# Optimization experiments

Hardware: AMD Instinct MI355X
Metric: run time of the kernel (lower is better)

Reference implementation:

```python
import jax, jax.numpy as jnp
import numpy as np

B, T, D = 16, 512, 1024
H = 4
DH = D // H
L = 2
FF = 4 * D
MAX_CORR = 3
THRESH = 0.3
EPS = 1e-5


def _ln(x, g, b):
    mu = x.mean(-1, keepdims=True)
    var = ((x - mu) ** 2).mean(-1, keepdims=True)
    return (x - mu) / jnp.sqrt(var + EPS) * g + b


def _prm(x, Wqkv, bqkv, Wo, bo, ln1_g, ln1_b, W1, b1, W2, b2, ln2_g, ln2_b,
         rh_W1, rh_b1, rh_W2, rh_b2):
    # PyTorch TransformerEncoder (post-LN, relu, dropout off) with causal mask
    Bs, Ts, _ = x.shape
    causal = jnp.triu(jnp.ones((Ts, Ts), dtype=bool), k=1)  # True = masked
    for l in range(L):
        qkv = x @ Wqkv[l].T + bqkv[l]  # (B,T,3D)
        q, k, v = jnp.split(qkv, 3, axis=-1)
        q = q.reshape(Bs, Ts, H, DH)
        k = k.reshape(Bs, Ts, H, DH)
        v = v.reshape(Bs, Ts, H, DH)
        scores = jnp.einsum('bthd,bshd->bhts', q, k) / jnp.sqrt(jnp.float32(DH))
        scores = jnp.where(causal[None, None], -jnp.inf, scores)
        attn = jax.nn.softmax(scores, axis=-1)
        o = jnp.einsum('bhts,bshd->bthd', attn, v).reshape(Bs, Ts, D)
        o = o @ Wo[l].T + bo[l]
        x = _ln(x + o, ln1_g[l], ln1_b[l])
        h = jax.nn.relu(x @ W1[l].T + b1[l]) @ W2[l].T + b2[l]
        x = _ln(x + h, ln2_g[l], ln2_b[l])
    r = jax.nn.relu(x @ rh_W1.T + rh_b1) @ rh_W2.T + rh_b2  # (B,T,1)
    return jax.nn.sigmoid(r[..., 0])  # (B,T)


def setup_inputs() -> dict:
    key = jax.random.key(0)
    ks = jax.random.split(key, 24)
    s = 0.02
    inp = {
        'chain': jax.random.normal(ks[0], (B, T, D), jnp.float32),
        'Wqkv': jax.random.normal(ks[1], (L, 3 * D, D), jnp.float32) * s,
        'bqkv': jnp.zeros((L, 3 * D), jnp.float32),
        'Wo': jax.random.normal(ks[2], (L, D, D), jnp.float32) * s,
        'bo': jnp.zeros((L, D), jnp.float32),
        'ln1_g': jnp.ones((L, D), jnp.float32),
        'ln1_b': jnp.zeros((L, D), jnp.float32),
        'W1': jax.random.normal(ks[3], (L, FF, D), jnp.float32) * s,
        'b1': jnp.zeros((L, FF), jnp.float32),
        'W2': jax.random.normal(ks[4], (L, D, FF), jnp.float32) * s,
        'b2': jnp.zeros((L, D), jnp.float32),
        'ln2_g': jnp.ones((L, D), jnp.float32),
        'ln2_b': jnp.zeros((L, D), jnp.float32),
        'rh_W1': jax.random.normal(ks[5], (D // 2, D), jnp.float32) * s,
        'rh_b1': jnp.zeros((D // 2,), jnp.float32),
        'rh_W2': jax.random.normal(ks[6], (1, D // 2), jnp.float32) * s,
        'rh_b2': jnp.full((1,), -1.0, jnp.float32),  # bias so some scores fall below threshold
        'cor_W1': jax.random.normal(ks[7], (2 * D, 2 * D), jnp.float32) * s,
        'cor_b1': jnp.zeros((2 * D,), jnp.float32),
        'cor_W2': jax.random.normal(ks[8], (D, 2 * D), jnp.float32) * s,
        'cor_b2': jnp.zeros((D,), jnp.float32),
    }
    return inp


def reference(chain, Wqkv, bqkv, Wo, bo, ln1_g, ln1_b, W1, b1, W2, b2,
              ln2_g, ln2_b, rh_W1, rh_b1, rh_W2, rh_b2,
              cor_W1, cor_b1, cor_W2, cor_b2):
    prm = lambda x: _prm(x, Wqkv, bqkv, Wo, bo, ln1_g, ln1_b, W1, b1, W2, b2,
                         ln2_g, ln2_b, rh_W1, rh_b1, rh_W2, rh_b2)
    scores0 = prm(chain)
    corrected = chain
    counts = jnp.zeros((B,), jnp.int32)
    offs = jnp.array([-1, 0, 1], jnp.int32)
    tpos = jnp.arange(T)
    for _ in range(MAX_CORR):
        s = prm(corrected)  # (B,T)
        below = s < THRESH
        has_bad = below.any(axis=-1)  # (B,)
        # worst = first argmin among below-threshold steps (matches torch argmin over gathered)
        w = jnp.argmin(jnp.where(below, s, jnp.inf), axis=-1)  # (B,)
        # context: mean over valid window [w-1, w+2)
        idxs = w[:, None] + offs  # (B,3)
        valid = (idxs >= 0) & (idxs < T)
        gathered = jnp.take_along_axis(corrected, jnp.clip(idxs, 0, T - 1)[..., None], axis=1)  # (B,3,D)
        ctx = (gathered * valid[..., None]).sum(1) / valid.sum(1, keepdims=True)  # (B,D)
        cur = jnp.take_along_axis(corrected, jnp.broadcast_to(w[:, None, None], (B, 1, D)), axis=1)[:, 0]  # (B,D)
        cinp = jnp.concatenate([cur, ctx], axis=-1)  # (B,2D)
        new_step = jax.nn.relu(cinp @ cor_W1.T + cor_b1) @ cor_W2.T + cor_b2  # (B,D)
        sel = (tpos[None, :] == w[:, None]) & has_bad[:, None]  # (B,T)
        corrected = jnp.where(sel[..., None], new_step[:, None, :], corrected)
        counts = counts + has_bad.astype(jnp.int32)
    final_scores = prm(corrected)
    improved = final_scores.mean(-1) > scores0.mean(-1)
    return corrected, counts, final_scores, improved
```

## Files before the change

### kernel.cpp

```cpp
#include <hip/hip_runtime.h>
#include <math.h>

#define B_ 16
#define T_ 512
#define D_ 1024
#define H_ 4
#define DH_ 256
#define FF_ 4096
#define M_ (B_*T_)
#define THRESH_ 0.3f
#define EPS_ 1e-5f

#define GF_RELU 1
#define GF_RES  2
#define GF_OUTBF16 4
#define GF_SPLITV 8

typedef unsigned short ushort_t;
typedef unsigned int uint_t;

using s16x8 = __attribute__((ext_vector_type(8))) short;
using f32x4 = __attribute__((ext_vector_type(4))) float;
using f32x16 = __attribute__((ext_vector_type(16))) float;

typedef const __attribute__((address_space(1))) void* gas_ptr;
typedef __attribute__((address_space(3))) void* lds_ptr;

static __device__ __forceinline__ ushort_t f2bf(float f) {
  uint_t x = __float_as_uint(f);
  return (ushort_t)((x + 0x7FFFu + ((x >> 16) & 1u)) >> 16);
}
static __device__ __forceinline__ float bf2f(ushort_t u) {
  return __uint_as_float(((uint_t)u) << 16);
}

__global__ __launch_bounds__(256)
void cvt_f32_bf16(const float* __restrict__ in, ushort_t* __restrict__ out, int n)
{
  const int i = (blockIdx.x * 256 + threadIdx.x) << 2;
  if (i >= n) return;
  const float4 v = *(const float4*)(in + i);
  ushort4 o;
  o.x = f2bf(v.x); o.y = f2bf(v.y); o.z = f2bf(v.z); o.w = f2bf(v.w);
  *(ushort4*)(out + i) = o;
}

__global__ __launch_bounds__(256)
void gemm_bf16(const ushort_t* __restrict__ A, const ushort_t* __restrict__ Bt,
               const float* __restrict__ bias, const ushort_t* __restrict__ res,
               float* __restrict__ outF, ushort_t* __restrict__ outB,
               ushort_t* __restrict__ vt,
               int M, int N, int K, int flags)
{
  __shared__ ushort_t As[128 * 32];
  __shared__ ushort_t Bs[128 * 32];
  const int npn = gridDim.x;
  const int pid = blockIdx.y * npn + blockIdx.x;
  const int group = 8 * npn;
  const int first_m = (pid / group) * 8;
  const int pid_m = first_m + (pid % 8);
  const int pid_n = (pid % group) >> 3;
  const int n0 = pid_n << 7;
  const int m0 = pid_m << 7;

  const int tid = threadIdx.x;
  const int wv = tid >> 6, ln = tid & 63;
  const int wm = (wv >> 1) << 6;
  const int wn = (wv & 1) << 6;
  const int col32 = ln & 31, l5 = ln >> 5;

  f32x16 acc[2][2] = {};

  const ushort_t* ga = A + (size_t)(m0 + wv * 16 + (ln >> 2)) * K + ((ln & 3) << 3);
  const ushort_t* gb = Bt + (size_t)(n0 + wv * 16 + (ln >> 2)) * K + ((ln & 3) << 3);
  ushort_t* lA = &As[wv * 512];
  ushort_t* lB = &Bs[wv * 512];

  for (int k0 = 0; k0 < K; k0 += 32) {
    __builtin_amdgcn_global_load_lds((gas_ptr)(const void*)ga,
                                     (lds_ptr)(void*)lA, 16, 0, 0);
    __builtin_amdgcn_global_load_lds((gas_ptr)(const void*)(ga + (size_t)64 * K),
                                     (lds_ptr)(void*)(lA + 2048), 16, 0, 0);
    __builtin_amdgcn_global_load_lds((gas_ptr)(const void*)gb,
                                     (lds_ptr)(void*)lB, 16, 0, 0);
    __builtin_amdgcn_global_load_lds((gas_ptr)(const void*)(gb + (size_t)64 * K),
                                     (lds_ptr)(void*)(lB + 2048), 16, 0, 0);
    ga += 32; gb += 32;
    __syncthreads();
    s16x8 af[2][2], bfr[2][2];
#pragma unroll
    for (int mt = 0; mt < 2; ++mt)
#pragma unroll
      for (int kh = 0; kh < 2; ++kh)
        af[mt][kh] = *(const s16x8*)(&As[(wm + mt * 32 + col32) * 32
                                         + kh * 16 + l5 * 8]);
#pragma unroll
    for (int nt = 0; nt < 2; ++nt)
#pragma unroll
      for (int kh = 0; kh < 2; ++kh)
        bfr[nt][kh] = *(const s16x8*)(&Bs[(wn + nt * 32 + col32) * 32
                                          + kh * 16 + l5 * 8]);
#pragma unroll
    for (int kh = 0; kh < 2; ++kh)
#pragma unroll
      for (int mt = 0; mt < 2; ++mt)
#pragma unroll
        for (int nt = 0; nt < 2; ++nt)
          acc[mt][nt] = __builtin_amdgcn_mfma_f32_32x32x16_bf16(
              af[mt][kh], bfr[nt][kh], acc[mt][nt], 0, 0, 0);
    __syncthreads();
  }

#pragma unroll
  for (int mt = 0; mt < 2; ++mt)
#pragma unroll
    for (int nt = 0; nt < 2; ++nt) {
      const int c = n0 + wn + nt * 32 + col32;
      const float bb = bias[c];
      const bool isV = (flags & GF_SPLITV) && (c >= 2048);
#pragma unroll
      for (int reg = 0; reg < 16; ++reg) {
        const int row = m0 + wm + mt * 32 + (reg & 3) + ((reg >> 2) << 3)
                        + (l5 << 2);
        float v = acc[mt][nt][reg] + bb;
        const size_t idx = (size_t)row * N + c;
        if (flags & GF_RES) v += bf2f(res[idx]);
        if (flags & GF_RELU) v = fmaxf(v, 0.f);
        if (isV) {
          const int t = row & 511, bb2 = row >> 9;
          const int hh = (c - 2048) >> 8, d = (c - 2048) & 255;
          vt[(((size_t)(bb2 * 4 + hh) * 16 + (t >> 5)) << 13) + d * 32 + (t & 31)]
              = f2bf(v);
        } else if (flags & GF_OUTBF16) outB[idx] = f2bf(v);
        else outF[idx] = v;
      }
    }
}

__global__ __launch_bounds__(256)
void flash_attn(const ushort_t* __restrict__ qkv, const ushort_t* __restrict__ vtg,
                ushort_t* __restrict__ ao)
{
  __shared__ ushort_t Ks[2][8 * 64 * 32];
  __shared__ ushort_t Vs[2][2 * 256 * 32];
  __shared__ ushort_t Ph[4][16][80];
  __shared__ ushort_t Pl[4][16][80];
  const int qt = (int)gridDim.x - 1 - blockIdx.x;
  const int t0 = qt << 6;
  const int bh = blockIdx.y;
  const int b = bh >> 2, h = bh & 3;
  const int nIter = qt + 1;
  const int tid = threadIdx.x;
  const int wv = tid >> 6, ln = tid & 63;
  const int lrow = ln & 15, quad = ln >> 4;

  s16x8 qf[8];
  {
    const ushort_t* qrow = qkv + (size_t)(b * T_ + t0 + wv * 16 + lrow) * 3072
                           + h * 256 + quad * 8;
#pragma unroll
    for (int kc = 0; kc < 8; ++kc)
      qf[kc] = *(const s16x8*)(qrow + kc * 32);
  }

  const ushort_t* kg = qkv + (size_t)(b * T_) * 3072 + 1024 + h * 256;
  const ushort_t* vg = vtg + (size_t)bh * 131072;

  auto issue_k = [&](int i, int buf) {
#pragma unroll
    for (int iss = 0; iss < 8; ++iss) {
      const int R = 128 * wv + 16 * iss + (ln >> 2);
      const ushort_t* g = kg + (size_t)(64 * i + (R & 63)) * 3072
                          + (R >> 6) * 32 + ((ln & 3) << 3);
      ushort_t* l = &Ks[buf][(128 * wv + 16 * iss) * 32];
      __builtin_amdgcn_global_load_lds((gas_ptr)(const void*)g,
                                       (lds_ptr)(void*)l, 16, 0, 0);
    }
  };
  auto issue_v = [&](int i, int buf) {
#pragma unroll
    for (int iss = 0; iss < 8; ++iss) {
      const ushort_t* g = vg + (size_t)i * 16384 + wv * 4096 + iss * 512 + ln * 8;
      ushort_t* l = &Vs[buf][wv * 4096 + iss * 512];
      __builtin_amdgcn_global_load_lds((gas_ptr)(const void*)g,
                                       (lds_ptr)(void*)l, 16, 0, 0);
    }
  };

  issue_k(0, 0);
  issue_v(0, 0);

  f32x4 o[16] = {};
  float Mx[4], L[4];
#pragma unroll
  for (int r = 0; r < 4; ++r) { Mx[r] = -3.0e38f; L[r] = 0.f; }

  for (int it = 0; it < nIter; ++it) {
    const int buf = it & 1;
    __syncthreads();
    if (it + 1 < nIter) { issue_k(it + 1, buf ^ 1); issue_v(it + 1, buf ^ 1); }

    f32x4 s[4] = {};
#pragma unroll
    for (int kc = 0; kc < 8; ++kc)
#pragma unroll
      for (int j = 0; j < 4; ++j) {
        const s16x8 bfv = *(const s16x8*)(&Ks[buf][(kc * 64 + 16 * j + lrow) * 32
                                                   + quad * 8]);
        s[j] = __builtin_amdgcn_mfma_f32_16x16x32_bf16(qf[kc], bfv, s[j], 0, 0, 0);
      }

    const bool diag = (it == qt);
#pragma unroll
    for (int j = 0; j < 4; ++j)
#pragma unroll
      for (int r = 0; r < 4; ++r) {
        float v = s[j][r] * 0.0625f;
        if (diag && (16 * j + lrow > 16 * wv + quad * 4 + r)) v = -INFINITY;
        s[j][r] = v;
      }

    float alpha[4];
#pragma unroll
    for (int r = 0; r < 4; ++r) {
      float m = fmaxf(fmaxf(s[0][r], s[1][r]), fmaxf(s[2][r], s[3][r]));
      m = fmaxf(m, __shfl_xor(m, 1));
      m = fmaxf(m, __shfl_xor(m, 2));
      m = fmaxf(m, __shfl_xor(m, 4));
      m = fmaxf(m, __shfl_xor(m, 8));
      const float mn = fmaxf(Mx[r], m);
      alpha[r] = __expf(Mx[r] - mn);
      Mx[r] = mn;
      float l = 0.f;
#pragma unroll
      for (int j = 0; j < 4; ++j) {
        const float p = __expf(s[j][r] - mn);
        s[j][r] = p;
        l += p;
      }
      l += __shfl_xor(l, 1);
      l += __shfl_xor(l, 2);
      l += __shfl_xor(l, 4);
      l += __shfl_xor(l, 8);
      L[r] = L[r] * alpha[r] + l;
    }

#pragma unroll
    for (int j = 0; j < 4; ++j)
#pragma unroll
      for (int r = 0; r < 4; ++r) {
        const float p = s[j][r];
        const ushort_t hi = f2bf(p);
        Ph[wv][quad * 4 + r][16 * j + lrow] = hi;
        Pl[wv][quad * 4 + r][16 * j + lrow] = f2bf(p - bf2f(hi));
      }
#pragma unroll
    for (int jd = 0; jd < 16; ++jd)
#pragma unroll
      for (int r = 0; r < 4; ++r)
        o[jd][r] *= alpha[r];

#pragma unroll
    for (int c = 0; c < 2; ++c) {
      const s16x8 ph = *(const s16x8*)(&Ph[wv][lrow][32 * c + quad * 8]);
      const s16x8 pl = *(const s16x8*)(&Pl[wv][lrow][32 * c + quad * 8]);
#pragma unroll
      for (int jd = 0; jd < 16; ++jd) {
        const s16x8 vb = *(const s16x8*)(&Vs[buf][(c * 256 + 16 * jd + lrow) * 32
                                                  + quad * 8]);
        o[jd] = __builtin_amdgcn_mfma_f32_16x16x32_bf16(ph, vb, o[jd], 0, 0, 0);
        o[jd] = __builtin_amdgcn_mfma_f32_16x16x32_bf16(pl, vb, o[jd], 0, 0, 0);
      }
    }
  }

  float inv[4];
#pragma unroll
  for (int r = 0; r < 4; ++r) inv[r] = 1.f / L[r];
  ushort_t* aob = ao + (size_t)(b * T_ + t0 + 16 * wv + quad * 4) * 1024 + h * 256;
#pragma unroll
  for (int jd = 0; jd < 16; ++jd)
#pragma unroll
    for (int r = 0; r < 4; ++r)
      aob[(size_t)r * 1024 + 16 * jd + lrow] = f2bf(o[jd][r] * inv[r]);
}

__global__ __launch_bounds__(256)
void gemm_bt(const float* __restrict__ A, const float* __restrict__ Bt,
             const float* __restrict__ bias, float* __restrict__ out,
             int M, int N, int K, int flags)
{
  __shared__ float As[16][68];
  __shared__ float Bs[16][68];
  const int n0 = blockIdx.x << 6;
  const int m0 = blockIdx.y << 6;
  const int tx = threadIdx.x, ty = threadIdx.y;
  const int tid = (ty << 4) + tx;
  const int lr = tid >> 2;
  const int lc = (tid & 3) << 2;
  float c[4][4] = {};
  for (int k0 = 0; k0 < K; k0 += 16) {
    float4 av = make_float4(0.f, 0.f, 0.f, 0.f);
    if (m0 + lr < M)
      av = *(const float4*)(A + (size_t)(m0 + lr) * K + k0 + lc);
    const float4 bv = *(const float4*)(Bt + (size_t)(n0 + lr) * K + k0 + lc);
    As[lc + 0][lr] = av.x; As[lc + 1][lr] = av.y;
    As[lc + 2][lr] = av.z; As[lc + 3][lr] = av.w;
    Bs[lc + 0][lr] = bv.x; Bs[lc + 1][lr] = bv.y;
    Bs[lc + 2][lr] = bv.z; Bs[lc + 3][lr] = bv.w;
    __syncthreads();
#pragma unroll
    for (int k = 0; k < 16; ++k) {
      const float4 a = *(const float4*)(&As[k][ty << 2]);
      const float4 b = *(const float4*)(&Bs[k][tx << 2]);
      c[0][0] += a.x*b.x; c[0][1] += a.x*b.y; c[0][2] += a.x*b.z; c[0][3] += a.x*b.w;
      c[1][0] += a.y*b.x; c[1][1] += a.y*b.y; c[1][2] += a.y*b.z; c[1][3] += a.y*b.w;
      c[2][0] += a.z*b.x; c[2][1] += a.z*b.y; c[2][2] += a.z*b.z; c[2][3] += a.z*b.w;
      c[3][0] += a.w*b.x; c[3][1] += a.w*b.y; c[3][2] += a.w*b.z; c[3][3] += a.w*b.w;
    }
    __syncthreads();
  }
  const int n = n0 + (tx << 2);
  const float4 bb = *(const float4*)(bias + n);
#pragma unroll
  for (int i = 0; i < 4; ++i) {
    const int m = m0 + (ty << 2) + i;
    if (m >= M) break;
    float4 v = make_float4(c[i][0] + bb.x, c[i][1] + bb.y,
                           c[i][2] + bb.z, c[i][3] + bb.w);
    if (flags & GF_RELU) {
      v.x = fmaxf(v.x, 0.f); v.y = fmaxf(v.y, 0.f);
      v.z = fmaxf(v.z, 0.f); v.w = fmaxf(v.w, 0.f);
    }
    *(float4*)(out + (size_t)m * N + n) = v;
  }
}

__global__ __launch_bounds__(256)
void layernorm_k(const float* __restrict__ in, const float* __restrict__ g,
                 const float* __restrict__ bta, ushort_t* __restrict__ outb)
{
  const int row = blockIdx.x;
  const int tid = threadIdx.x;
  const int wave = tid >> 6, lane = tid & 63;
  const float4 v = *(const float4*)(in + (size_t)row * D_ + (tid << 2));
  float s = v.x + v.y + v.z + v.w;
  float ss = v.x*v.x + v.y*v.y + v.z*v.z + v.w*v.w;
  for (int off = 32; off; off >>= 1) {
    s  += __shfl_down(s, off, 64);
    ss += __shfl_down(ss, off, 64);
  }
  __shared__ float ra[4], rb[4];
  if (!lane) { ra[wave] = s; rb[wave] = ss; }
  __syncthreads();
  s  = ra[0] + ra[1] + ra[2] + ra[3];
  ss = rb[0] + rb[1] + rb[2] + rb[3];
  const float mu = s * (1.f / (float)D_);
  const float var = ss * (1.f / (float)D_) - mu * mu;
  const float rstd = rsqrtf(var + EPS_);
  const float4 gv = *(const float4*)(g + (tid << 2));
  const float4 bv = *(const float4*)(bta + (tid << 2));
  ushort4 o;
  o.x = f2bf((v.x - mu) * rstd * gv.x + bv.x);
  o.y = f2bf((v.y - mu) * rstd * gv.y + bv.y);
  o.z = f2bf((v.z - mu) * rstd * gv.z + bv.z);
  o.w = f2bf((v.w - mu) * rstd * gv.w + bv.w);
  *(ushort4*)(outb + (size_t)row * D_ + (tid << 2)) = o;
}

__global__ __launch_bounds__(256)
void head2_sigmoid(const float* __restrict__ h1, const float* __restrict__ w2,
                   const float* __restrict__ b2, float* __restrict__ sout)
{
  const int tid = threadIdx.x;
  const int wave = tid >> 6, lane = tid & 63;
  const int m = (blockIdx.x << 2) + wave;
  const float* hr = h1 + (size_t)m * 512;
  float s = 0.f;
#pragma unroll
  for (int i = 0; i < 8; ++i) s += hr[i * 64 + lane] * w2[i * 64 + lane];
  for (int off = 32; off; off >>= 1) s += __shfl_down(s, off, 64);
  if (!lane) sout[m] = 1.f / (1.f + expf(-(s + b2[0])));
}

__global__ __launch_bounds__(256)
void select_worst(const float* __restrict__ s, int* __restrict__ w,
                  int* __restrict__ hasbad, int* __restrict__ counts)
{
  const int b = blockIdx.x, tid = threadIdx.x;
  const float* sr = s + b * T_;
  float bv = INFINITY; int bi = 0;
  for (int i = tid; i < T_; i += 256) {
    const float v = sr[i];
    const float cand = (v < THRESH_) ? v : INFINITY;
    if (cand < bv || (cand == bv && i < bi)) { bv = cand; bi = i; }
  }
  __shared__ float rv[256];
  __shared__ int ri[256];
  rv[tid] = bv; ri[tid] = bi;
  __syncthreads();
  for (int str = 128; str; str >>= 1) {
    if (tid < str) {
      const float v2 = rv[tid + str]; const int i2 = ri[tid + str];
      if (v2 < rv[tid] || (v2 == rv[tid] && i2 < ri[tid])) { rv[tid] = v2; ri[tid] = i2; }
    }
    __syncthreads();
  }
  if (!tid) {
    const int bad = (rv[0] < INFINITY) ? 1 : 0;
    w[b] = ri[0];
    hasbad[b] = bad;
    counts[b] += bad;
  }
}

__global__ __launch_bounds__(256)
void gather_cinp(const float* __restrict__ corr, const int* __restrict__ w,
                 float* __restrict__ cinp)
{
  const int b = blockIdx.x, tid = threadIdx.x;
  const int wi = w[b];
  const float* base = corr + (size_t)b * T_ * D_;
  const int nv = 3 - (wi == 0 ? 1 : 0) - (wi == T_ - 1 ? 1 : 0);
  const float inv = 1.f / (float)nv;
  const int d = tid << 2;
  const float4 cur = *(const float4*)(base + (size_t)wi * D_ + d);
  float4 acc = cur;
  if (wi > 0) {
    const float4 p = *(const float4*)(base + (size_t)(wi - 1) * D_ + d);
    acc.x += p.x; acc.y += p.y; acc.z += p.z; acc.w += p.w;
  }
  if (wi < T_ - 1) {
    const float4 p = *(const float4*)(base + (size_t)(wi + 1) * D_ + d);
    acc.x += p.x; acc.y += p.y; acc.z += p.z; acc.w += p.w;
  }
  acc.x *= inv; acc.y *= inv; acc.z *= inv; acc.w *= inv;
  *(float4*)(cinp + (size_t)b * (2 * D_) + d) = cur;
  *(float4*)(cinp + (size_t)b * (2 * D_) + D_ + d) = acc;
}

__global__ __launch_bounds__(256)
void apply_corr(float* __restrict__ corr, const int* __restrict__ w,
                const int* __restrict__ hasbad, const float* __restrict__ ns)
{
  const int b = blockIdx.x;
  if (!hasbad[b]) return;
  const int wi = w[b], tid = threadIdx.x;
  *(float4*)(corr + (size_t)(b * T_ + wi) * D_ + (tid << 2)) =
      *(const float4*)(ns + (size_t)b * D_ + (tid << 2));
}

__global__ __launch_bounds__(256)
void init_copy(const float* __restrict__ chain, float* __restrict__ corr,
               int* __restrict__ counts)
{
  const size_t i = ((size_t)blockIdx.x * 256 + threadIdx.x) << 2;
  *(float4*)(corr + i) = *(const float4*)(chain + i);
  if (blockIdx.x == 0 && threadIdx.x < B_) counts[threadIdx.x] = 0;
}

__global__ __launch_bounds__(256)
void finalize_k(const float* __restrict__ s0, const float* __restrict__ fs,
                const int* __restrict__ cnt, float* __restrict__ oc,
                float* __restrict__ oi)
{
  const int b = blockIdx.x, tid = threadIdx.x;
  const int wave = tid >> 6, lane = tid & 63;
  float a = s0[b * T_ + tid] + s0[b * T_ + tid + 256];
  float c = fs[b * T_ + tid] + fs[b * T_ + tid + 256];
  for (int off = 32; off; off >>= 1) {
    a += __shfl_down(a, off, 64);
    c += __shfl_down(c, off, 64);
  }
  __shared__ float ra[4], rc[4];
  if (!lane) { ra[wave] = a; rc[wave] = c; }
  __syncthreads();
  if (!tid) {
    const float as = ra[0] + ra[1] + ra[2] + ra[3];
    const float cs = rc[0] + rc[1] + rc[2] + rc[3];
    oc[b] = (float)cnt[b];
    oi[b] = (cs > as) ? 1.f : 0.f;
  }
}

extern "C" void kernel_launch(void* const* d_in, const int* in_sizes, int n_in,
                              void* d_out, int out_size, void* d_ws, size_t ws_size,
                              hipStream_t stream)
{
  const float* chain  = (const float*)d_in[0];
  const float* Wqkv   = (const float*)d_in[1];
  const float* bqkv   = (const float*)d_in[2];
  const float* Wo     = (const float*)d_in[3];
  const float* bo     = (const float*)d_in[4];
  const float* ln1g   = (const float*)d_in[5];
  const float* ln1b   = (const float*)d_in[6];
  const float* W1     = (const float*)d_in[7];
  const float* b1     = (const float*)d_in[8];
  const float* W2     = (const float*)d_in[9];
  const float* b2     = (const float*)d_in[10];
  const float* ln2g   = (const float*)d_in[11];
  const float* ln2b   = (const float*)d_in[12];
  const float* rhW1   = (const float*)d_in[13];
  const float* rhb1   = (const float*)d_in[14];
  const float* rhW2   = (const float*)d_in[15];
  const float* rhb2   = (const float*)d_in[16];
  const float* corW1  = (const float*)d_in[17];
  const float* corb1  = (const float*)d_in[18];
  const float* corW2  = (const float*)d_in[19];
  const float* corb2  = (const float*)d_in[20];

  float* ws = (float*)d_ws;
  ushort_t* QKV16 = (ushort_t*)ws;
  float*    PRE   = ws;
  float*    E     = ws;
  ushort_t* Hb    = (ushort_t*)(ws + 12582912);
  ushort_t* Vtg   = (ushort_t*)(ws + 12582912);
  ushort_t* Xb    = (ushort_t*)(ws + 29360128);
  ushort_t* AOb   = (ushort_t*)(ws + 33554432);
  float*    HH    = ws + 33554432;
  float*    cinp  = ws + 33554432;
  float*    corrH = cinp + 32768;
  float*    nstep = corrH + 32768;
  ushort_t* W16     = (ushort_t*)(ws + 37748736);
  ushort_t* Wqkv16  = W16;
  ushort_t* Wo16    = W16 + 6291456;
  ushort_t* W116    = W16 + 8388608;
  ushort_t* W216    = W16 + 16777216;
  ushort_t* rhW116  = W16 + 25165824;
  float* s0buf = ws + 50593792;
  float* sbuf  = s0buf + 8192;
  int* wbuf   = (int*)(sbuf + 8192);
  int* badbuf = wbuf + 16;
  int* cntbuf = badbuf + 16;

  float* outCorr   = (float*)d_out;
  float* outCounts = outCorr + 8388608;
  float* outFS     = outCounts + 16;
  float* outImpr   = outFS + 8192;

  const dim3 blk2(16, 16);
  const dim3 blk1(256);

  cvt_f32_bf16<<<dim3(6144), blk1, 0, stream>>>(Wqkv, Wqkv16, 6291456);
  cvt_f32_bf16<<<dim3(2048), blk1, 0, stream>>>(Wo,   Wo16,   2097152);
  cvt_f32_bf16<<<dim3(8192), blk1, 0, stream>>>(W1,   W116,   8388608);
  cvt_f32_bf16<<<dim3(8192), blk1, 0, stream>>>(W2,   W216,   8388608);
  cvt_f32_bf16<<<dim3(512),  blk1, 0, stream>>>(rhW1, rhW116, 524288);

  auto run_prm = [&](const float* xin, float* scoresOut) {
    cvt_f32_bf16<<<dim3(8192), blk1, 0, stream>>>(xin, Xb, 8388608);
    for (int l = 0; l < 2; ++l) {
      gemm_bf16<<<dim3(24, 64), blk1, 0, stream>>>(
          Xb, Wqkv16 + (size_t)l * 3 * D_ * D_, bqkv + (size_t)l * 3 * D_,
          nullptr, nullptr, QKV16, Vtg, M_, 3 * D_, D_,
          GF_OUTBF16 | GF_SPLITV);
      flash_attn<<<dim3(8, 64), blk1, 0, stream>>>(QKV16, Vtg, AOb);
      gemm_bf16<<<dim3(8, 64), blk1, 0, stream>>>(
          AOb, Wo16 + (size_t)l * D_ * D_, bo + (size_t)l * D_,
          Xb, PRE, nullptr, nullptr, M_, D_, D_, GF_RES);
      layernorm_k<<<dim3(M_), blk1, 0, stream>>>(PRE, ln1g + l * D_,
                                                 ln1b + l * D_, Xb);
      gemm_bf16<<<dim3(32, 64), blk1, 0, stream>>>(
          Xb, W116 + (size_t)l * FF_ * D_, b1 + (size_t)l * FF_,
          nullptr, nullptr, Hb, nullptr, M_, FF_, D_, GF_RELU | GF_OUTBF16);
      gemm_bf16<<<dim3(8, 64), blk1, 0, stream>>>(
          Hb, W216 + (size_t)l * D_ * FF_, b2 + (size_t)l * D_,
          Xb, E, nullptr, nullptr, M_, D_, FF_, GF_RES);
      layernorm_k<<<dim3(M_), blk1, 0, stream>>>(E, ln2g + l * D_,
                                                 ln2b + l * D_, Xb);
    }
    gemm_bf16<<<dim3(4, 64), blk1, 0, stream>>>(
        Xb, rhW116, rhb1, nullptr, HH, nullptr, nullptr, M_, 512, D_, GF_RELU);
    head2_sigmoid<<<dim3(M_ / 4), blk1, 0, stream>>>(HH, rhW2, rhb2, scoresOut);
  };

  auto run_iter = [&](const float* sPtr) {
    select_worst<<<dim3(B_), blk1, 0, stream>>>(sPtr, wbuf, badbuf, cntbuf);
    gather_cinp<<<dim3(B_), blk1, 0, stream>>>(outCorr, wbuf, cinp);
    gemm_bt<<<dim3(32, 1), blk2, 0, stream>>>(cinp, corW1, corb1, corrH,
                                              B_, 2 * D_, 2 * D_, GF_RELU);
    gemm_bt<<<dim3(16, 1), blk2, 0, stream>>>(corrH, corW2, corb2, nstep,
                                              B_, D_, 2 * D_, 0);
    apply_corr<<<dim3(B_), blk1, 0, stream>>>(outCorr, wbuf, badbuf, nstep);
  };

  init_copy<<<dim3(8192), blk1, 0, stream>>>(chain, outCorr, cntbuf);

  run_prm(chain, s0buf);
  run_iter(s0buf);
  run_prm(outCorr, sbuf);
  run_iter(sbuf);
  run_prm(outCorr, sbuf);
  run_iter(sbuf);
  run_prm(outCorr, outFS);
  finalize_k<<<dim3(B_), blk1, 0, stream>>>(s0buf, outFS, cntbuf,
                                            outCounts, outImpr);
  (void)in_sizes; (void)n_in; (void)out_size; (void)ws_size;
}
```

Measured before the change: 5.136 ms.

## Double GEMM K-tile to 64 and XOR-swizzle LDS layout to avoid bank conflicts

The bf16 GEMM now stages 64-wide K slices per iteration instead of 32, halving the number of barrier pairs per K loop. The LDS tile is stored with an XOR swizzle on 16-byte chunks, applied both in the global-to-LDS load addresses and in the fragment reads, to reduce LDS bank conflicts on the MFMA operand loads. LDS use per block doubles to 32 KB, which may lower occupancy.

```diff
diff --git a/kernel.cpp b/kernel.cpp
--- a/kernel.cpp
+++ b/kernel.cpp
@@ -52,8 +52,8 @@
                ushort_t* __restrict__ vt,
                int M, int N, int K, int flags)
 {
-  __shared__ ushort_t As[128 * 32];
-  __shared__ ushort_t Bs[128 * 32];
+  __shared__ ushort_t As[128 * 64];
+  __shared__ ushort_t Bs[128 * 64];
   const int npn = gridDim.x;
   const int pid = blockIdx.y * npn + blockIdx.x;
   const int group = 8 * npn;
@@ -71,43 +71,46 @@
 
   f32x16 acc[2][2] = {};
 
-  const ushort_t* ga = A + (size_t)(m0 + wv * 16 + (ln >> 2)) * K + ((ln & 3) << 3);
-  const ushort_t* gb = Bt + (size_t)(n0 + wv * 16 + (ln >> 2)) * K + ((ln & 3) << 3);
-  ushort_t* lA = &As[wv * 512];
-  ushort_t* lB = &Bs[wv * 512];
-
-  for (int k0 = 0; k0 < K; k0 += 32) {
-    __builtin_amdgcn_global_load_lds((gas_ptr)(const void*)ga,
-                                     (lds_ptr)(void*)lA, 16, 0, 0);
-    __builtin_amdgcn_global_load_lds((gas_ptr)(const void*)(ga + (size_t)64 * K),
-                                     (lds_ptr)(void*)(lA + 2048), 16, 0, 0);
-    __builtin_amdgcn_global_load_lds((gas_ptr)(const void*)gb,
-                                     (lds_ptr)(void*)lB, 16, 0, 0);
-    __builtin_amdgcn_global_load_lds((gas_ptr)(const void*)(gb + (size_t)64 * K),
-                                     (lds_ptr)(void*)(lB + 2048), 16, 0, 0);
-    ga += 32; gb += 32;
+  const int srow = (ln >> 3);
+  const int schunk = (ln & 7) ^ srow;
+  const ushort_t* gaBase = A + (size_t)(m0 + wv * 32 + srow) * K + schunk * 8;
+  const ushort_t* gbBase = Bt + (size_t)(n0 + wv * 32 + srow) * K + schunk * 8;
+  ushort_t* lA = &As[wv * 2048];
+  ushort_t* lB = &Bs[wv * 2048];
+
+  for (int k0 = 0; k0 < K; k0 += 64) {
+#pragma unroll
+    for (int iss = 0; iss < 4; ++iss) {
+      __builtin_amdgcn_global_load_lds(
+          (gas_ptr)(const void*)(gaBase + (size_t)(iss * 8) * K + k0),
+          (lds_ptr)(void*)(lA + iss * 512), 16, 0, 0);
+      __builtin_amdgcn_global_load_lds(
+          (gas_ptr)(const void*)(gbBase + (size_t)(iss * 8) * K + k0),
+          (lds_ptr)(void*)(lB + iss * 512), 16, 0, 0);
+    }
     __syncthreads();
-    s16x8 af[2][2], bfr[2][2];
-#pragma unroll
-    for (int mt = 0; mt < 2; ++mt)
-#pragma unroll
-      for (int kh = 0; kh < 2; ++kh)
-        af[mt][kh] = *(const s16x8*)(&As[(wm + mt * 32 + col32) * 32
-                                         + kh * 16 + l5 * 8]);
-#pragma unroll
-    for (int nt = 0; nt < 2; ++nt)
-#pragma unroll
-      for (int kh = 0; kh < 2; ++kh)
-        bfr[nt][kh] = *(const s16x8*)(&Bs[(wn + nt * 32 + col32) * 32
-                                          + kh * 16 + l5 * 8]);
-#pragma unroll
-    for (int kh = 0; kh < 2; ++kh)
+#pragma unroll
+    for (int kh = 0; kh < 4; ++kh) {
+      s16x8 af[2], bfr[2];
+#pragma unroll
+      for (int mt = 0; mt < 2; ++mt) {
+        const int row = wm + mt * 32 + col32;
+        const int pos = ((kh << 1) + l5) ^ (col32 & 7);
+        af[mt] = *(const s16x8*)(&As[row * 64 + pos * 8]);
+      }
+#pragma unroll
+      for (int nt = 0; nt < 2; ++nt) {
+        const int row = wn + nt * 32 + col32;
+        const int pos = ((kh << 1) + l5) ^ (col32 & 7);
+        bfr[nt] = *(const s16x8*)(&Bs[row * 64 + pos * 8]);
+      }
 #pragma unroll
       for (int mt = 0; mt < 2; ++mt)
 #pragma unroll
         for (int nt = 0; nt < 2; ++nt)
           acc[mt][nt] = __builtin_amdgcn_mfma_f32_32x32x16_bf16(
-              af[mt][kh], bfr[nt][kh], acc[mt][nt], 0, 0, 0);
+              af[mt], bfr[nt], acc[mt][nt], 0, 0, 0);
+    }
     __syncthreads();
   }
 
```

After: 4.612 ms. -10.2%, faster.
